# Kernel optimization log

Hardware: AMD Instinct MI355X
Metric: run time of the kernel (lower is better)

Reference implementation:

```python
import jax, jax.numpy as jnp
import numpy as np

IN_FEATURES = 256
OUT_FEATURES = 4096
BATCH = 8192


def _build_expansion_mapping():
    # out_feature j is a copy of in_feature j // (OUT_FEATURES // IN_FEATURES)
    k = OUT_FEATURES // IN_FEATURES
    em = np.zeros((OUT_FEATURES, IN_FEATURES), dtype=np.float32)
    em[np.arange(OUT_FEATURES), np.arange(OUT_FEATURES) // k] = 1.0
    return jnp.asarray(em)


def setup_inputs() -> dict:
    key = jax.random.key(0)
    x = jax.random.normal(key, (BATCH, IN_FEATURES), dtype=jnp.float32)
    return {
        "x": x,
        "expansion_mapping": _build_expansion_mapping(),
        "means": jnp.zeros((OUT_FEATURES,), dtype=jnp.float32),
        "vars_": jnp.ones((OUT_FEATURES,), dtype=jnp.float32),
        "coefs": jnp.ones((OUT_FEATURES,), dtype=jnp.float32),
    }


def reference(x, expansion_mapping, means, vars_, coefs):
    # (E @ x^T)^T == x @ E^T : [B, F_out]
    xe = jnp.einsum('bi,oi->bo', x, expansion_mapping)
    z = (xe - means) / vars_
    return jnp.exp(-0.5 * z * z) * coefs
```

## Files before the change

### kernel.cpp

```cpp
#include <hip/hip_runtime.h>
#include <hip/hip_bf16.h>

#define IN_F 256
#define OUT_F 4096
#define BATCH 8192

__global__ __launch_bounds__(256) void urbf_build_idx(
    const float* __restrict__ em, int* __restrict__ idx) {
    const int wave = blockIdx.x * (blockDim.x >> 6) + (threadIdx.x >> 6);
    const int lane = threadIdx.x & 63;
    if (wave >= OUT_F) return;
    const float* row = em + (size_t)wave * IN_F;
    int found = 0;
    #pragma unroll
    for (int c = 0; c < IN_F; c += 64) {
        const float v = row[c + lane];
        const unsigned long long m = __ballot(v != 0.0f);
        if (m) found = c + (int)(__ffsll((unsigned long long)m) - 1);
    }
    if (lane == 0) idx[wave] = found;
}

__global__ __launch_bounds__(256) void urbf_main(
    const float* __restrict__ x, const int* __restrict__ idx,
    const float* __restrict__ means, const float* __restrict__ vars_,
    const float* __restrict__ coefs, float* __restrict__ out) {
    const int g = blockIdx.x * blockDim.x + threadIdx.x;
    const int b  = g >> 10;
    const int j4 = g & 1023;
    const int j  = j4 << 2;

    const int4   si = *(const int4*)(idx + j);
    const float4 mu = *(const float4*)(means + j);
    const float4 vv = *(const float4*)(vars_ + j);
    const float4 cc = *(const float4*)(coefs + j);

    const float* xrow = x + (size_t)b * IN_F;
    const float x0 = xrow[si.x];
    const float x1 = xrow[si.y];
    const float x2 = xrow[si.z];
    const float x3 = xrow[si.w];

    float4 o;
    float z;
    z = (x0 - mu.x) / vv.x; o.x = __expf(-0.5f * z * z) * cc.x;
    z = (x1 - mu.y) / vv.y; o.y = __expf(-0.5f * z * z) * cc.y;
    z = (x2 - mu.z) / vv.z; o.z = __expf(-0.5f * z * z) * cc.z;
    z = (x3 - mu.w) / vv.w; o.w = __expf(-0.5f * z * z) * cc.w;

    *(float4*)(out + ((size_t)g << 2)) = o;
}

extern "C" void kernel_launch(void* const* d_in, const int* in_sizes, int n_in,
                              void* d_out, int out_size, void* d_ws, size_t ws_size,
                              hipStream_t stream) {
    const float* x     = (const float*)d_in[0];
    const float* em    = (const float*)d_in[1];
    const float* means = (const float*)d_in[2];
    const float* vars_ = (const float*)d_in[3];
    const float* coefs = (const float*)d_in[4];
    float* out = (float*)d_out;
    int* idx = (int*)d_ws;

    urbf_build_idx<<<OUT_F / 4, 256, 0, stream>>>(em, idx);

    const int total4 = BATCH * OUT_F / 4;
    urbf_main<<<total4 / 256, 256, 0, stream>>>(x, idx, means, vars_, coefs, out);
}
```

Baseline: 175.6 us.

## Loop over batch rows per thread, precompute exp2 coefficient, use nontemporal stores

Each thread now keeps its column's index, mean, variance-derived coefficient and coef in registers and loops over 16 batch rows, instead of reloading the per-column parameters for every output vector. The divide and exp are folded into one precomputed scale per column so each element costs one exp2 call. Output is written with nontemporal stores to avoid polluting cache with the large write stream. Per-thread work grows and the grid shrinks, which lowers the parallelism available to hide latency, and the reciprocal-based math can differ slightly from exact division.

```diff
diff --git a/kernel.cpp b/kernel.cpp
--- a/kernel.cpp
+++ b/kernel.cpp
@@ -4,6 +4,9 @@
 #define IN_F 256
 #define OUT_F 4096
 #define BATCH 8192
+#define B_PER_BLOCK 16
+
+typedef float v4f __attribute__((ext_vector_type(4)));
 
 __global__ __launch_bounds__(256) void urbf_build_idx(
     const float* __restrict__ em, int* __restrict__ idx) {
@@ -25,9 +28,7 @@
     const float* __restrict__ x, const int* __restrict__ idx,
     const float* __restrict__ means, const float* __restrict__ vars_,
     const float* __restrict__ coefs, float* __restrict__ out) {
-    const int g = blockIdx.x * blockDim.x + threadIdx.x;
-    const int b  = g >> 10;
-    const int j4 = g & 1023;
+    const int j4 = blockIdx.x * 256 + threadIdx.x;
     const int j  = j4 << 2;
 
     const int4   si = *(const int4*)(idx + j);
@@ -35,20 +36,34 @@
     const float4 vv = *(const float4*)(vars_ + j);
     const float4 cc = *(const float4*)(coefs + j);
 
-    const float* xrow = x + (size_t)b * IN_F;
-    const float x0 = xrow[si.x];
-    const float x1 = xrow[si.y];
-    const float x2 = xrow[si.z];
-    const float x3 = xrow[si.w];
+    const float C = -0.72134752044448170368f;
+    float4 a;
+    {
+        float4 r;
+        r.x = __frcp_rn(vv.x); r.y = __frcp_rn(vv.y);
+        r.z = __frcp_rn(vv.z); r.w = __frcp_rn(vv.w);
+        a.x = C * r.x * r.x; a.y = C * r.y * r.y;
+        a.z = C * r.z * r.z; a.w = C * r.w * r.w;
+    }
 
-    float4 o;
-    float z;
-    z = (x0 - mu.x) / vv.x; o.x = __expf(-0.5f * z * z) * cc.x;
-    z = (x1 - mu.y) / vv.y; o.y = __expf(-0.5f * z * z) * cc.y;
-    z = (x2 - mu.z) / vv.z; o.z = __expf(-0.5f * z * z) * cc.z;
-    z = (x3 - mu.w) / vv.w; o.w = __expf(-0.5f * z * z) * cc.w;
+    const int b0 = blockIdx.y * B_PER_BLOCK;
+    #pragma unroll 4
+    for (int bb = 0; bb < B_PER_BLOCK; ++bb) {
+        const int b = b0 + bb;
+        const float* xrow = x + (size_t)b * IN_F;
+        const float x0 = xrow[si.x];
+        const float x1 = xrow[si.y];
+        const float x2 = xrow[si.z];
+        const float x3 = xrow[si.w];
 
-    *(float4*)(out + ((size_t)g << 2)) = o;
+        v4f o; float d;
+        d = x0 - mu.x; o.x = exp2f(d * d * a.x) * cc.x;
+        d = x1 - mu.y; o.y = exp2f(d * d * a.y) * cc.y;
+        d = x2 - mu.z; o.z = exp2f(d * d * a.z) * cc.z;
+        d = x3 - mu.w; o.w = exp2f(d * d * a.w) * cc.w;
+
+        __builtin_nontemporal_store(o, (v4f*)(out + (size_t)b * OUT_F + j));
+    }
 }
 
 extern "C" void kernel_launch(void* const* d_in, const int* in_sizes, int n_in,
@@ -64,6 +79,6 @@
 
     urbf_build_idx<<<OUT_F / 4, 256, 0, stream>>>(em, idx);
 
-    const int total4 = BATCH * OUT_F / 4;
-    urbf_main<<<total4 / 256, 256, 0, stream>>>(x, idx, means, vars_, coefs, out);
+    dim3 grid(OUT_F / 4 / 256, BATCH / B_PER_BLOCK);
+    urbf_main<<<grid, 256, 0, stream>>>(x, idx, means, vars_, coefs, out);
 }
```

Result: faster. 162.8 us (-7.3%).
